# Kernel optimization log

Hardware: AMD Instinct MI355X
Metric: run time of the kernel (lower is better)

The kernel has to match this reference:

```python
import jax, jax.numpy as jnp
import numpy as np

TOPK = 13
ALPHA = 1.0
BETA = 6.0
CENTER_RADIUS = 0.5
EPS = 1e-7
IMG = 2048
STRIDES = (8, 16, 32)


def _make_anchor_points():
    pts = []
    for s in STRIDES:
        n = IMG // s
        c = (jnp.arange(n, dtype=jnp.float32) + 0.5) * s
        yy, xx = jnp.meshgrid(c, c, indexing='ij')
        pts.append(jnp.stack([xx.ravel(), yy.ravel()], axis=-1))
    return jnp.concatenate(pts, axis=0)  # [86016, 2]


def setup_inputs() -> dict:
    key = jax.random.key(0)
    k = jax.random.split(key, 6)
    anchor_points = _make_anchor_points()           # [P, 2]
    P = anchor_points.shape[0]
    C, G = 365, 100
    pred_scores = jax.random.normal(k[0], (P, C), dtype=jnp.float32) * 2.0 - 2.0
    pred_objectness = jax.random.normal(k[1], (P,), dtype=jnp.float32)
    # predicted boxes: anchor +- positive ltrb distances (valid xyxy)
    dist = jax.random.uniform(k[2], (P, 4), minval=2.0, maxval=120.0, dtype=jnp.float32)
    pred_boxes = jnp.concatenate([anchor_points - dist[:, :2], anchor_points + dist[:, 2:]], axis=-1)
    ctr = jax.random.uniform(k[3], (G, 2), minval=64.0, maxval=IMG - 64.0, dtype=jnp.float32)
    half = jax.random.uniform(k[4], (G, 2), minval=16.0, maxval=160.0, dtype=jnp.float32)
    gt_boxes = jnp.concatenate([ctr - half, ctr + half], axis=-1)  # [G, 4] xyxy
    gt_labels = jax.random.randint(k[5], (G,), 0, C, dtype=jnp.int64)
    valid_class_mask = jnp.ones((C,), dtype=bool)
    return {
        'pred_scores': pred_scores,
        'pred_boxes': pred_boxes,
        'pred_objectness': pred_objectness,
        'anchor_points': anchor_points,
        'gt_boxes': gt_boxes,
        'gt_labels': gt_labels,
        'valid_class_mask': valid_class_mask,
    }


def _iou_matrix(gt_boxes, pred_boxes):
    # gt: [G,4], pred: [P,4] -> [G,P]
    lt = jnp.maximum(gt_boxes[:, None, :2], pred_boxes[None, :, :2])
    rb = jnp.minimum(gt_boxes[:, None, 2:], pred_boxes[None, :, 2:])
    wh = jnp.clip(rb - lt, 0.0)
    inter = wh[..., 0] * wh[..., 1]
    area_g = jnp.prod(jnp.clip(gt_boxes[:, 2:] - gt_boxes[:, :2], 0.0), axis=-1)
    area_p = jnp.prod(jnp.clip(pred_boxes[:, 2:] - pred_boxes[:, :2], 0.0), axis=-1)
    union = area_g[:, None] + area_p[None, :] - inter
    return inter / (union + EPS)


def reference(pred_scores, pred_boxes, pred_objectness, anchor_points, gt_boxes, gt_labels, valid_class_mask):
    P, C = pred_scores.shape
    G = gt_boxes.shape[0]
    gt_labels = gt_labels.astype(jnp.int32)

    valid_gt = (gt_labels >= 0) & (gt_labels < C) & valid_class_mask[jnp.clip(gt_labels, 0, C - 1)]

    # inside-box mask [G, P]
    ax, ay = anchor_points[:, 0], anchor_points[:, 1]
    inside = ((ax[None, :] >= gt_boxes[:, 0:1]) & (ax[None, :] <= gt_boxes[:, 2:3]) &
              (ay[None, :] >= gt_boxes[:, 1:2]) & (ay[None, :] <= gt_boxes[:, 3:4]))

    gt_center = (gt_boxes[:, :2] + gt_boxes[:, 2:]) * 0.5               # [G,2]
    half_size = jnp.clip((gt_boxes[:, 2:] - gt_boxes[:, :2]) * 0.5, 1.0)
    center_delta = jnp.abs(anchor_points[None, :, :] - gt_center[:, None, :]) / half_size[:, None, :]  # [G,P,2]
    cd_max = center_delta.max(axis=-1)                                   # [G,P]
    center_mask = cd_max <= CENTER_RADIUS

    strict = inside & center_mask
    has_center = strict.any(axis=1, keepdims=True)                       # [G,1]
    cand = jnp.where(has_center, strict, inside)                         # fallback to inside-only

    iou = _iou_matrix(gt_boxes, pred_boxes)                              # [G,P]
    cls_scores = jax.nn.sigmoid(pred_scores[:, jnp.clip(gt_labels, 0, C - 1)].T)  # [G,P]
    pred_obj = jax.nn.sigmoid(pred_objectness)                           # [P]
    quality = jnp.sqrt(jnp.clip(pred_obj[None, :] * cls_scores, 0.0))
    center_prior = jnp.exp(-0.5 * jnp.sum(center_delta ** 2, axis=-1))   # [G,P]
    align = (quality ** ALPHA) * (iou ** BETA) * center_prior            # [G,P], >= 0

    masked = jnp.where(cand & valid_gt[:, None], align, -1.0)
    top_val, top_idx = jax.lax.top_k(masked, TOPK)                       # [G,TOPK]
    # scatter per-GT top-k back to [G,P]; entries with value -1 (non-candidates) stay excluded
    sel = jnp.full((G, P), -1.0, dtype=align.dtype)
    sel = sel.at[jnp.arange(G)[:, None], top_idx].set(jnp.where(top_val > -0.5, top_val, -1.0))

    # sequential 'override only if strictly greater' == per-point argmax with ties to earliest GT
    metric = sel.max(axis=0)                                             # [P]
    best_gt = jnp.argmax(sel, axis=0)                                    # [P]
    fg_mask = metric > -0.5

    overlap = iou[best_gt, jnp.arange(P)]                                # [P]
    matched_gt_indices = jnp.where(fg_mask, best_gt, -1)
    matched_labels = jnp.where(fg_mask, gt_labels[best_gt], -1)

    target_boxes = jnp.where(fg_mask[:, None], gt_boxes[best_gt], 0.0)   # [P,4]
    lab_idx = jnp.clip(matched_labels, 0, C - 1)
    score_val = jnp.where(fg_mask, jnp.clip(overlap, 0.1), 0.0)
    target_scores = jnp.zeros((P, C), dtype=pred_scores.dtype).at[jnp.arange(P), lab_idx].set(score_val)

    return (target_scores, target_boxes, fg_mask, matched_gt_indices, matched_labels)
```

## Files before the change

kernel.cpp:

```cpp
#include <hip/hip_runtime.h>
#include <cstdint>
#include <cstddef>

#define TOPK 13
#define MAXC 2816
#define NLEV 3
#define NZB  1792

__global__ __launch_bounds__(256) void pdl_zero_topk_kernel(
    const float*  __restrict__ scores,
    const float4* __restrict__ pboxes,
    const float*  __restrict__ obj,
    const float4* __restrict__ gtb,
    const int*    __restrict__ glab,
    const unsigned char* __restrict__ vmask,
    unsigned long long* __restrict__ ws_keys,
    float* __restrict__ out,
    int C, int G, long long nfloat4)
{
    const int bid = blockIdx.x;
    const int tid = threadIdx.x;

    if (bid >= G) {
        float4* dst = (float4*)out;
        const float4 z = make_float4(0.0f, 0.0f, 0.0f, 0.0f);
        const long long chunk = (nfloat4 + NZB - 1) / NZB;
        long long s0 = (long long)(bid - G) * chunk;
        long long s1 = s0 + chunk; if (s1 > nfloat4) s1 = nfloat4;
        for (long long i = s0 + tid; i < s1; i += 1024) {
            dst[i] = z;
            if (i + 256 < s1) dst[i + 256] = z;
            if (i + 512 < s1) dst[i + 512] = z;
            if (i + 768 < s1) dst[i + 768] = z;
        }
        return;
    }

    const int g = bid;
    if (tid < TOPK) ws_keys[g * TOPK + tid] = 0ULL;

    const float4 gb = gtb[g];
    const int lab = glab[g];
    bool valid = (lab >= 0) && (lab < C);
    if (valid) {
        valid = (vmask[lab] != 0) || (vmask[4 * (size_t)lab] != 0) ||
                (vmask[8 * (size_t)lab] != 0);
    }
    if (!valid) return;

    __shared__ int s_flag;
    __shared__ int s_count;
    __shared__ unsigned long long s_wred[4];
    __shared__ unsigned long long s_keys[MAXC];

    if (tid == 0) { s_flag = 0; s_count = 0; }

    const float cx = (gb.x + gb.z) * 0.5f;
    const float cy = (gb.y + gb.w) * 0.5f;
    const float hx = fmaxf((gb.z - gb.x) * 0.5f, 1.0f);
    const float hy = fmaxf((gb.w - gb.y) * 0.5f, 1.0f);
    const float area_g = fmaxf(gb.z - gb.x, 0.0f) * fmaxf(gb.w - gb.y, 0.0f);

    const int ls[NLEV]   = {8, 16, 32};
    const int ln[NLEV]   = {256, 128, 64};
    const int loff[NLEV] = {0, 65536, 81920};
    int x0[NLEV], y0[NLEV], ww[NLEV], cnt[NLEV];
    int T = 0;
    #pragma unroll
    for (int l = 0; l < NLEV; ++l) {
        const float fs = (float)ls[l];
        int xa = (int)floorf(gb.x / fs - 0.5f);
        int xb = (int)ceilf (gb.z / fs - 0.5f);
        int ya = (int)floorf(gb.y / fs - 0.5f);
        int yb = (int)ceilf (gb.w / fs - 0.5f);
        xa = xa > 0 ? xa : 0;
        ya = ya > 0 ? ya : 0;
        xb = xb < ln[l] - 1 ? xb : ln[l] - 1;
        yb = yb < ln[l] - 1 ? yb : ln[l] - 1;
        int w = xb - xa + 1; if (w < 0) w = 0;
        int h = yb - ya + 1; if (h < 0) h = 0;
        x0[l] = xa; y0[l] = ya; ww[l] = w;
        cnt[l] = w * h;
        T += cnt[l];
    }
    __syncthreads();

    bool any_strict = false;
    for (int j = tid; j < T; j += 256) {
        int jj = j, l = 0;
        if (jj >= cnt[0]) { jj -= cnt[0]; l = 1; if (jj >= cnt[1]) { jj -= cnt[1]; l = 2; } }
        const int iy = jj / ww[l];
        const int ix = jj - iy * ww[l];
        const float fs = (float)ls[l];
        const float ax = ((float)(x0[l] + ix) + 0.5f) * fs;
        const float ay = ((float)(y0[l] + iy) + 0.5f) * fs;
        if (ax >= gb.x && ax <= gb.z && ay >= gb.y && ay <= gb.w) {
            const float cdx = fabsf(ax - cx) / hx;
            const float cdy = fabsf(ay - cy) / hy;
            if (fmaxf(cdx, cdy) <= 0.5f) any_strict = true;
        }
    }
    if (any_strict) s_flag = 1;
    __syncthreads();
    const bool has_center = (s_flag != 0);

    for (int j = tid; j < T; j += 256) {
        int jj = j, l = 0;
        if (jj >= cnt[0]) { jj -= cnt[0]; l = 1; if (jj >= cnt[1]) { jj -= cnt[1]; l = 2; } }
        const int iy = jj / ww[l];
        const int ix = jj - iy * ww[l];
        const float fs = (float)ls[l];
        const float ax = ((float)(x0[l] + ix) + 0.5f) * fs;
        const float ay = ((float)(y0[l] + iy) + 0.5f) * fs;
        if (!(ax >= gb.x && ax <= gb.z && ay >= gb.y && ay <= gb.w)) continue;
        const float cdx = fabsf(ax - cx) / hx;
        const float cdy = fabsf(ay - cy) / hy;
        const bool strict = fmaxf(cdx, cdy) <= 0.5f;
        if (has_center && !strict) continue;

        const int p = loff[l] + (y0[l] + iy) * ln[l] + (x0[l] + ix);
        const float4 pb = pboxes[p];
        const float so = 1.0f / (1.0f + expf(-obj[p]));
        const float sc = 1.0f / (1.0f + expf(-scores[(size_t)p * C + lab]));
        const float prior = expf(-0.5f * (cdx * cdx + cdy * cdy));
        const float ltx = fmaxf(gb.x, pb.x);
        const float lty = fmaxf(gb.y, pb.y);
        const float rbx = fminf(gb.z, pb.z);
        const float rby = fminf(gb.w, pb.w);
        const float wi = fmaxf(rbx - ltx, 0.0f);
        const float hi = fmaxf(rby - lty, 0.0f);
        const float inter = wi * hi;
        const float area_p = fmaxf(pb.z - pb.x, 0.0f) * fmaxf(pb.w - pb.y, 0.0f);
        const float iou = inter / (area_g + area_p - inter + 1e-7f);
        const float q = sqrtf(fmaxf(so * sc, 0.0f));
        const float i2 = iou * iou;
        const float align = q * (i2 * i2 * i2) * prior;

        const unsigned long long key =
            ((unsigned long long)__float_as_uint(align) << 32)
          | (unsigned long long)(0xFFFFFFFFu ^ (unsigned)p);
        const int slot = atomicAdd(&s_count, 1);
        if (slot < MAXC) s_keys[slot] = key;
    }
    __syncthreads();
    const int M = s_count < MAXC ? s_count : MAXC;

    for (int r = 0; r < TOPK; ++r) {
        unsigned long long best = 0ULL; int bi = -1;
        for (int i = tid; i < M; i += 256) {
            const unsigned long long k = s_keys[i];
            if (k > best) { best = k; bi = i; }
        }
        unsigned long long wb = best;
        #pragma unroll
        for (int d = 32; d >= 1; d >>= 1) {
            const unsigned long long o = __shfl_xor(wb, d, 64);
            if (o > wb) wb = o;
        }
        if ((tid & 63) == 0) s_wred[tid >> 6] = wb;
        __syncthreads();
        unsigned long long winner = s_wred[0];
        if (s_wred[1] > winner) winner = s_wred[1];
        if (s_wred[2] > winner) winner = s_wred[2];
        if (s_wred[3] > winner) winner = s_wred[3];
        if (winner == 0ULL) break;
        if (best == winner) s_keys[bi] = 0ULL;
        if (tid == 0) ws_keys[g * TOPK + r] = winner;
        __syncthreads();
    }
}

__global__ __launch_bounds__(256) void pdl_finalize_kernel(
    const float4* __restrict__ pboxes,
    const float4* __restrict__ gtb,
    const int*    __restrict__ glab,
    const unsigned long long* __restrict__ ws_keys,
    float* __restrict__ out,
    int P, int C, int G)
{
    const int tid = threadIdx.x;
    const int p0  = blockIdx.x * 256;
    const int p   = p0 + tid;

    __shared__ unsigned long long s_best[256];
    s_best[tid] = 0ULL;
    __syncthreads();

    const int npairs = G * TOPK;
    for (int j = tid; j < npairs; j += 256) {
        const unsigned long long k = ws_keys[j];
        if (k == 0ULL) continue;
        const unsigned pp = 0xFFFFFFFFu ^ (unsigned)(k & 0xFFFFFFFFull);
        const int d = (int)pp - p0;
        if (d >= 0 && d < 256) {
            const int g = j / TOPK;
            const unsigned long long key2 =
                (k & 0xFFFFFFFF00000000ull) |
                (unsigned long long)(0xFFFFFFFFu - (unsigned)g);
            atomicMax(&s_best[d], key2);
        }
    }
    __syncthreads();

    if (p < P) {
        const unsigned long long k = s_best[tid];
        const bool fg = (k != 0ULL);
        float4 tb = make_float4(0.0f, 0.0f, 0.0f, 0.0f);
        float mgi = -1.0f, mlab = -1.0f;
        if (fg) {
            const int bg = (int)(0xFFFFFFFFu - (unsigned)(k & 0xFFFFFFFFull));
            const float4 gbx = gtb[bg];
            const float4 pb  = pboxes[p];
            const float ltx = fmaxf(gbx.x, pb.x);
            const float lty = fmaxf(gbx.y, pb.y);
            const float rbx = fminf(gbx.z, pb.z);
            const float rby = fminf(gbx.w, pb.w);
            const float wi = fmaxf(rbx - ltx, 0.0f);
            const float hi = fmaxf(rby - lty, 0.0f);
            const float inter = wi * hi;
            const float ag = fmaxf(gbx.z - gbx.x, 0.0f) * fmaxf(gbx.w - gbx.y, 0.0f);
            const float ap = fmaxf(pb.z - pb.x, 0.0f) * fmaxf(pb.w - pb.y, 0.0f);
            const float iou = inter / (ag + ap - inter + 1e-7f);
            const int lb = glab[bg];
            tb   = gbx;
            mgi  = (float)bg;
            mlab = (float)lb;
            int lbc = lb < 0 ? 0 : (lb > C - 1 ? C - 1 : lb);
            out[(size_t)p * C + lbc] = fmaxf(iou, 0.1f);
        }
        float4* boxes_out = (float4*)(out + (size_t)P * C);
        boxes_out[p] = tb;
        const size_t base = (size_t)P * C + (size_t)4 * P;
        out[base + p]                 = fg ? 1.0f : 0.0f;
        out[base + (size_t)P + p]     = mgi;
        out[base + (size_t)2 * P + p] = mlab;
    }
}

extern "C" void kernel_launch(void* const* d_in, const int* in_sizes, int n_in,
                              void* d_out, int out_size, void* d_ws, size_t ws_size,
                              hipStream_t stream)
{
    (void)n_in; (void)out_size; (void)ws_size;

    const float*  scores = (const float*)d_in[0];
    const float4* pboxes = (const float4*)d_in[1];
    const float*  obj    = (const float*)d_in[2];
    const float4* gtb    = (const float4*)d_in[4];
    const int*    glab   = (const int*)d_in[5];
    const unsigned char* vmask = (const unsigned char*)d_in[6];

    const int P = in_sizes[2];
    const int C = in_sizes[0] / P;
    const int G = in_sizes[5];

    unsigned long long* ws_keys = (unsigned long long*)d_ws;
    float* out = (float*)d_out;

    const long long nfloat4 = ((long long)P * C) / 4;

    pdl_zero_topk_kernel<<<G + NZB, 256, 0, stream>>>(scores, pboxes, obj, gtb,
                                                      glab, vmask, ws_keys, out,
                                                      C, G, nfloat4);
    pdl_finalize_kernel<<<(P + 255) / 256, 256, 0, stream>>>(pboxes, gtb, glab,
                                                             ws_keys, out, P, C, G);
}
```

Baseline: 37.49 us.

## Replace block-wide top-k rounds with per-wave top-k and final merge

Each wave now extracts its own top-13 keys independently using only shuffles, with no block barriers per round. Only the owning thread rescans its strided slice after a key is removed. A single wave then merges the 4x13 candidates into the final top-13. The number of zero-fill blocks is also raised, which changes the split between zeroing and top-k work.

```diff
diff --git a/kernel.cpp b/kernel.cpp
--- a/kernel.cpp
+++ b/kernel.cpp
@@ -5,7 +5,7 @@
 #define TOPK 13
 #define MAXC 2816
 #define NLEV 3
-#define NZB  1792
+#define NZB  1948
 
 __global__ __launch_bounds__(256) void pdl_zero_topk_kernel(
     const float*  __restrict__ scores,
@@ -50,7 +50,7 @@
 
     __shared__ int s_flag;
     __shared__ int s_count;
-    __shared__ unsigned long long s_wred[4];
+    __shared__ unsigned long long s_merge[4 * TOPK];
     __shared__ unsigned long long s_keys[MAXC];
 
     if (tid == 0) { s_flag = 0; s_count = 0; }
@@ -145,28 +145,45 @@
     __syncthreads();
     const int M = s_count < MAXC ? s_count : MAXC;
 
+    const int wid  = tid >> 6;
+    const int lane = tid & 63;
+
+    unsigned long long best = 0ULL; int bi = -1;
+    for (int i = tid; i < M; i += 256) {
+        const unsigned long long k = s_keys[i];
+        if (k > best) { best = k; bi = i; }
+    }
     for (int r = 0; r < TOPK; ++r) {
-        unsigned long long best = 0ULL; int bi = -1;
-        for (int i = tid; i < M; i += 256) {
-            const unsigned long long k = s_keys[i];
-            if (k > best) { best = k; bi = i; }
-        }
         unsigned long long wb = best;
         #pragma unroll
         for (int d = 32; d >= 1; d >>= 1) {
             const unsigned long long o = __shfl_xor(wb, d, 64);
             if (o > wb) wb = o;
         }
-        if ((tid & 63) == 0) s_wred[tid >> 6] = wb;
-        __syncthreads();
-        unsigned long long winner = s_wred[0];
-        if (s_wred[1] > winner) winner = s_wred[1];
-        if (s_wred[2] > winner) winner = s_wred[2];
-        if (s_wred[3] > winner) winner = s_wred[3];
-        if (winner == 0ULL) break;
-        if (best == winner) s_keys[bi] = 0ULL;
-        if (tid == 0) ws_keys[g * TOPK + r] = winner;
-        __syncthreads();
+        if (lane == 0) s_merge[wid * TOPK + r] = wb;
+        if (wb != 0ULL && best == wb) {
+            s_keys[bi] = 0ULL;
+            best = 0ULL; bi = -1;
+            for (int i = tid; i < M; i += 256) {
+                const unsigned long long k = s_keys[i];
+                if (k > best) { best = k; bi = i; }
+            }
+        }
+    }
+    __syncthreads();
+
+    if (wid == 0) {
+        unsigned long long v = (lane < 4 * TOPK) ? s_merge[lane] : 0ULL;
+        for (int r = 0; r < TOPK; ++r) {
+            unsigned long long wb = v;
+            #pragma unroll
+            for (int d = 32; d >= 1; d >>= 1) {
+                const unsigned long long o = __shfl_xor(wb, d, 64);
+                if (o > wb) wb = o;
+            }
+            if (lane == 0) ws_keys[g * TOPK + r] = wb;
+            if (v == wb) v = 0ULL;
+        }
     }
 }
 
```

Measured after the change: 38.98 us. +4.0%, slower.
